# Kernel tuning notes

Measured on AMD Instinct MI355X. Metric: run time of the kernel, lower is better.

Reference implementation:

```python
import jax, jax.numpy as jnp
import numpy as np

D_MODEL = 256
N_LAYERS = 6
N_HEADS = 8
D_FF = 1024
HEAD_DIM = D_MODEL // N_HEADS
EPS = 1e-5


def layer_norm(x, scale, bias):
    mu = jnp.mean(x, axis=-1, keepdims=True)
    var = jnp.var(x, axis=-1, keepdims=True)
    return (x - mu) * jax.lax.rsqrt(var + EPS) * scale + bias


def setup_inputs() -> dict:
    key = jax.random.key(0)
    ks = jax.random.split(key, 12)
    B, T = 4, 2048
    x = jax.random.normal(ks[0], (B, T, D_MODEL), dtype=jnp.float32)
    L = N_LAYERS
    s = 0.02
    inp = {
        "x": x,
        "ln1_s": jnp.ones((L, D_MODEL), jnp.float32),
        "ln1_b": jnp.zeros((L, D_MODEL), jnp.float32),
        "wq": jax.random.normal(ks[1], (L, D_MODEL, D_MODEL), jnp.float32) * s,
        "bq": jnp.zeros((L, D_MODEL), jnp.float32),
        "wk": jax.random.normal(ks[2], (L, D_MODEL, D_MODEL), jnp.float32) * s,
        "bk": jnp.zeros((L, D_MODEL), jnp.float32),
        "wv": jax.random.normal(ks[3], (L, D_MODEL, D_MODEL), jnp.float32) * s,
        "bv": jnp.zeros((L, D_MODEL), jnp.float32),
        "wo": jax.random.normal(ks[4], (L, D_MODEL, D_MODEL), jnp.float32) * s,
        "bo": jnp.zeros((L, D_MODEL), jnp.float32),
        "ln2_s": jnp.ones((L, D_MODEL), jnp.float32),
        "ln2_b": jnp.zeros((L, D_MODEL), jnp.float32),
        "w1": jax.random.normal(ks[5], (L, D_MODEL, D_FF), jnp.float32) * s,
        "b1": jnp.zeros((L, D_FF), jnp.float32),
        "w2": jax.random.normal(ks[6], (L, D_FF, D_MODEL), jnp.float32) * s,
        "b2": jnp.zeros((L, D_MODEL), jnp.float32),
    }
    return inp


def reference(x, ln1_s, ln1_b, wq, bq, wk, bk, wv, bv, wo, bo, ln2_s, ln2_b, w1, b1, w2, b2):
    B, T, D = x.shape
    scale = 1.0 / jnp.sqrt(jnp.float32(HEAD_DIM))
    for l in range(N_LAYERS):
        normed = layer_norm(x, ln1_s[l], ln1_b[l])
        q = (normed @ wq[l] + bq[l]).reshape(B, T, N_HEADS, HEAD_DIM)
        k = (normed @ wk[l] + bk[l]).reshape(B, T, N_HEADS, HEAD_DIM)
        v = (normed @ wv[l] + bv[l]).reshape(B, T, N_HEADS, HEAD_DIM)
        scores = jnp.einsum('bqhd,bkhd->bhqk', q, k) * scale  # [B,H,T,T]
        attn = jax.nn.softmax(scores, axis=-1)
        attn_out = jnp.einsum('bhqk,bkhd->bqhd', attn, v).reshape(B, T, D)
        x = x + attn_out @ wo[l] + bo[l]
        h = layer_norm(x, ln2_s[l], ln2_b[l])
        h = jax.nn.gelu(h @ w1[l] + b1[l], approximate=False)
        x = x + h @ w2[l] + b2[l]
    return x
```

## Files before the change

### kernel.cpp

```cpp
#include <hip/hip_runtime.h>
#include <math.h>

#define D_MODELC 256
#define N_LAYERSC 6
#define N_HEADSC 8
#define D_FFC 1024
#define HEAD_DIMC 32
#define B_SZ 4
#define T_SEQ 2048
#define M_ROWS 8192
#define QKV_N 768
#define KSPLIT 2

typedef short bf16x8 __attribute__((ext_vector_type(8)));
typedef short bf16x4 __attribute__((ext_vector_type(4)));
typedef float f32x4  __attribute__((ext_vector_type(4)));
typedef unsigned u32x4 __attribute__((ext_vector_type(4)));
typedef unsigned short u16;

#define QSCALE 0.25503488f

#define SWZ(b) ((b) ^ (((b) >> 3) & 0x70))

__device__ __forceinline__ void gload16(const void* g, void* l) {
    __builtin_amdgcn_global_load_lds(
        (const __attribute__((address_space(1))) void*)g,
        (__attribute__((address_space(3))) void*)l, 16, 0, 0);
}

__device__ __forceinline__ u16 f2bf(float x) {
    unsigned u = __builtin_bit_cast(unsigned, x);
    u += 0x7FFF + ((u >> 16) & 1);
    return (u16)(u >> 16);
}

__device__ __forceinline__ float bf2f(short x) {
    return __builtin_bit_cast(float, (unsigned)((u16)x) << 16);
}

__device__ __forceinline__ unsigned pack2bf(float a, float b) {
    return __builtin_amdgcn_perm(__builtin_bit_cast(unsigned, b),
                                 __builtin_bit_cast(unsigned, a), 0x07060302u);
}

__device__ __forceinline__ float fast_gelu(float x) {
    float y  = x * 0.70710678118654752f;
    float ay = __builtin_fabsf(y);
    float t  = __builtin_amdgcn_rcpf(1.0f + 0.3275911f * ay);
    float p  = t * (0.254829592f + t * (-0.284496736f + t * (1.421413741f
               + t * (-1.453152027f + t * 1.061405429f))));
    float e  = __builtin_amdgcn_exp2f(-ay * ay * 1.4426950408889634f);
    float er = 1.0f - p * e;
    er = y < 0.0f ? -er : er;
    return 0.5f * x * (1.0f + er);
}

__device__ __forceinline__ void transpose_tile(
    const float* __restrict__ src, u16* __restrict__ dst,
    int K, int N, int k0, int n0, float scale, float (*ts)[33])
{
    const int r = threadIdx.x >> 3, c4 = (threadIdx.x & 7) * 4;
    const float4 v = *(const float4*)(src + (size_t)(k0 + r) * N + n0 + c4);
    ts[r][c4 + 0] = v.x; ts[r][c4 + 1] = v.y;
    ts[r][c4 + 2] = v.z; ts[r][c4 + 3] = v.w;
    __syncthreads();
    bf16x4 o;
#pragma unroll
    for (int i = 0; i < 4; i++) o[i] = (short)f2bf(ts[c4 + i][r] * scale);
    *(bf16x4*)(dst + (size_t)(n0 + r) * K + k0 + c4) = o;
}

__global__ __launch_bounds__(256) void prep_all(
    const float* __restrict__ wq, const float* __restrict__ wk,
    const float* __restrict__ wv, const float* __restrict__ wo,
    const float* __restrict__ w1, const float* __restrict__ w2,
    const float* __restrict__ bq, const float* __restrict__ bk,
    const float* __restrict__ bv,
    u16* __restrict__ wqkv_t, u16* __restrict__ wo_t,
    u16* __restrict__ w1_t, u16* __restrict__ w2_t,
    float* __restrict__ qkvb,
    const float* __restrict__ x, const float* __restrict__ gamma,
    const float* __restrict__ beta, float* __restrict__ X,
    u16* __restrict__ Y)
{
    __shared__ float ts[32][33];
    const int bid = blockIdx.x;
    if (bid < 1152) {
        const int sec = bid / 384, t = bid % 384;
        const int z = t >> 6, rem = t & 63, ty = rem >> 3, tx = rem & 7;
        const float* src = sec == 0 ? wq : (sec == 1 ? wk : wv);
        transpose_tile(src + (size_t)z * 65536,
                       wqkv_t + (size_t)z * QKV_N * 256 + sec * 256 * 256,
                       256, 256, ty * 32, tx * 32,
                       sec == 0 ? QSCALE : 1.0f, ts);
    } else if (bid < 1536) {
        const int t = bid - 1152;
        const int z = t >> 6, rem = t & 63, ty = rem >> 3, tx = rem & 7;
        transpose_tile(wo + (size_t)z * 65536, wo_t + (size_t)z * 65536,
                       256, 256, ty * 32, tx * 32, 1.0f, ts);
    } else if (bid < 3072) {
        const int t = bid - 1536;
        const int z = t >> 8, rem = t & 255, ty = rem >> 5, tx = rem & 31;
        transpose_tile(w1 + (size_t)z * 262144, w1_t + (size_t)z * 262144,
                       256, D_FFC, ty * 32, tx * 32, 1.0f, ts);
    } else if (bid < 4608) {
        const int t = bid - 3072;
        const int z = t >> 8, rem = t & 255, ty = rem >> 3, tx = rem & 7;
        transpose_tile(w2 + (size_t)z * 262144, w2_t + (size_t)z * 262144,
                       D_FFC, 256, ty * 32, tx * 32, 1.0f, ts);
    } else if (bid < 4626) {
        const int i = (bid - 4608) * 256 + threadIdx.x;
        const int l = i / QKV_N, j = i % QKV_N;
        float v;
        if (j < 256)      v = bq[l * 256 + j] * QSCALE;
        else if (j < 512) v = bk[l * 256 + j - 256];
        else              v = bv[l * 256 + j - 512];
        qkvb[i] = v;
    } else {
        const int w = threadIdx.x >> 6, lane = threadIdx.x & 63;
        const int row = (bid - 4626) * 4 + w;
        const float4 v = *(const float4*)(x + (size_t)row * 256 + lane * 4);
        *(float4*)(X + (size_t)row * 256 + lane * 4) = v;
        float sum = v.x + v.y + v.z + v.w;
        float sq  = v.x * v.x + v.y * v.y + v.z * v.z + v.w * v.w;
#pragma unroll
        for (int off = 32; off > 0; off >>= 1) {
            sum += __shfl_xor(sum, off, 64);
            sq  += __shfl_xor(sq,  off, 64);
        }
        float mu  = sum * (1.0f / 256.0f);
        float var = sq * (1.0f / 256.0f) - mu * mu;
        float rr  = rsqrtf(var + 1e-5f);
        const float4 g  = *(const float4*)(gamma + lane * 4);
        const float4 bb = *(const float4*)(beta + lane * 4);
        bf16x4 o;
        o[0] = (short)f2bf((v.x - mu) * rr * g.x + bb.x);
        o[1] = (short)f2bf((v.y - mu) * rr * g.y + bb.y);
        o[2] = (short)f2bf((v.z - mu) * rr * g.z + bb.z);
        o[3] = (short)f2bf((v.w - mu) * rr * g.w + bb.w);
        *(bf16x4*)(Y + (size_t)row * 256 + lane * 4) = o;
    }
}

template <int EPI>
__global__ __launch_bounds__(256) void mfma_gemm(
    const u16* __restrict__ A, const u16* __restrict__ Bt,
    const float* __restrict__ bias, u16* __restrict__ Vout,
    void* __restrict__ Cout, int N, int K)
{
    __shared__ u16 As[128 * 64];
    __shared__ u16 Bs[64 * 64];
    const int tid = threadIdx.x, w = tid >> 6, lane = tid & 63;
    const int c = lane & 15, quad = lane >> 4;
    const int row0 = blockIdx.y * 128, col0 = blockIdx.x * 64;
    const int wr = w >> 1, wc = w & 1;
    const int cswz = (c & 7) << 4;

    int flvA[4], rA[4], colA[4];
#pragma unroll
    for (int ci = 0; ci < 4; ci++) {
        flvA[ci] = (w * 4 + ci) * 1024 + lane * 16;
        const int fsw = SWZ(flvA[ci]);
        rA[ci]   = fsw >> 7;
        colA[ci] = (fsw & 127) >> 1;
    }
    int flvB[2], rB[2], colB[2];
#pragma unroll
    for (int ci = 0; ci < 2; ci++) {
        flvB[ci] = (w * 2 + ci) * 1024 + lane * 16;
        const int fsw = SWZ(flvB[ci]);
        rB[ci]   = fsw >> 7;
        colB[ci] = (fsw & 127) >> 1;
    }

    f32x4 acc[4][2] = {};

    for (int k0 = 0; k0 < K; k0 += 64) {
        __syncthreads();
#pragma unroll
        for (int ci = 0; ci < 4; ci++)
            gload16(A + (size_t)(row0 + rA[ci]) * K + k0 + colA[ci],
                    (char*)As + flvA[ci]);
#pragma unroll
        for (int ci = 0; ci < 2; ci++)
            gload16(Bt + (size_t)(col0 + rB[ci]) * K + k0 + colB[ci],
                    (char*)Bs + flvB[ci]);
        __syncthreads();
#pragma unroll
        for (int kk = 0; kk < 2; kk++) {
            bf16x8 af[4], bfv[2];
#pragma unroll
            for (int i = 0; i < 4; i++)
                af[i] = *(const bf16x8*)((const char*)As +
                    ((((wr * 64 + i * 16 + c) * 64 + kk * 32 + quad * 8) * 2) ^ cswz));
#pragma unroll
            for (int j = 0; j < 2; j++)
                bfv[j] = *(const bf16x8*)((const char*)Bs +
                    ((((wc * 32 + j * 16 + c) * 64 + kk * 32 + quad * 8) * 2) ^ cswz));
#pragma unroll
            for (int i = 0; i < 4; i++)
#pragma unroll
                for (int j = 0; j < 2; j++)
                    acc[i][j] = __builtin_amdgcn_mfma_f32_16x16x32_bf16(
                        af[i], bfv[j], acc[i][j], 0, 0, 0);
        }
    }

    float bj[2];
#pragma unroll
    for (int j = 0; j < 2; j++) bj[j] = bias[col0 + wc * 32 + j * 16 + c];

    if (EPI == 3 && col0 >= 512) {
#pragma unroll
        for (int i = 0; i < 4; i++) {
            const int tok = row0 + wr * 64 + i * 16 + quad * 4;
#pragma unroll
            for (int j = 0; j < 2; j++) {
                const int dim = col0 - 512 + wc * 32 + j * 16 + c;
                bf16x4 o;
#pragma unroll
                for (int r = 0; r < 4; r++) o[r] = (short)f2bf(acc[i][j][r] + bj[j]);
                *(bf16x4*)&Vout[(size_t)dim * M_ROWS + tok] = o;
            }
        }
        return;
    }

#pragma unroll
    for (int i = 0; i < 4; i++) {
#pragma unroll
        for (int r = 0; r < 4; r++) {
            const int gr = row0 + wr * 64 + i * 16 + quad * 4 + r;
#pragma unroll
            for (int j = 0; j < 2; j++) {
                const int gc = col0 + wc * 32 + j * 16 + c;
                float v = acc[i][j][r] + bj[j];
                if (EPI == 2) v = fast_gelu(v);
                ((u16*)Cout)[(size_t)gr * N + gc] = f2bf(v);
            }
        }
    }
}

template <int DOLN, int MERGE>
__global__ __launch_bounds__(256) void gemm_ln(
    const u16* __restrict__ A, const float* __restrict__ Lmrg,
    const u16* __restrict__ Bt, const float* __restrict__ bias,
    const float* __restrict__ resid, float* __restrict__ Xout,
    const float* __restrict__ gamma, const float* __restrict__ beta,
    u16* __restrict__ Nout, int K)
{
    __shared__ u16 As[16 * 64];
    __shared__ u16 Bs[256 * 64];
    __shared__ float2 red[4][16];
    const int tid = threadIdx.x, w = tid >> 6, lane = tid & 63;
    const int c = lane & 15, quad = lane >> 4;
    const int row0 = blockIdx.x * 16;
    const int cswz = (c & 7) << 4;

    const int flA  = tid * 16;
    const bool doA = tid < 128;
    const int fsA  = SWZ(flA);
    const int rA_m = flA >> 7, colA_m = (flA & 127) >> 1;
    const int rA_g = fsA >> 7, colA_g = (fsA & 127) >> 1;

    int flB[8], rB[8], colB[8];
#pragma unroll
    for (int ci = 0; ci < 8; ci++) {
        flB[ci]  = (w * 8 + ci) * 1024 + lane * 16;
        const int fsB = SWZ(flB[ci]);
        rB[ci]   = fsB >> 7;
        colB[ci] = (fsB & 127) >> 1;
    }

    f32x4 acc[4] = {};

    auto loadA = [&](int gc) -> bf16x8 {
        const int row = row0 + rA_m;
        const int head = gc >> 5;
        float ls = 0.f;
#pragma unroll
        for (int p = 0; p < KSPLIT; p++)
            ls += Lmrg[(size_t)p * M_ROWS * 8 + (size_t)row * 8 + head];
        const float inv = __builtin_amdgcn_rcpf(ls);
        float s[8] = {0.f, 0.f, 0.f, 0.f, 0.f, 0.f, 0.f, 0.f};
#pragma unroll
        for (int p = 0; p < KSPLIT; p++) {
            bf16x8 a = *(const bf16x8*)(A + (size_t)p * M_ROWS * 256
                                          + (size_t)row * 256 + gc);
#pragma unroll
            for (int j = 0; j < 8; j++) s[j] += bf2f(a[j]);
        }
        bf16x8 o;
#pragma unroll
        for (int j = 0; j < 8; j++) o[j] = (short)f2bf(s[j] * inv);
        return o;
    };

    bf16x8 pA;
    if (MERGE && doA) pA = loadA(colA_m);

    for (int k0 = 0; k0 < K; k0 += 64) {
        __syncthreads();
#pragma unroll
        for (int ci = 0; ci < 8; ci++)
            gload16(Bt + (size_t)rB[ci] * K + k0 + colB[ci], (char*)Bs + flB[ci]);
        if (MERGE) {
            if (doA) *(bf16x8*)((char*)As + fsA) = pA;
        } else {
            if (doA) gload16(A + (size_t)(row0 + rA_g) * K + k0 + colA_g,
                             (char*)As + flA);
        }
        __syncthreads();
        if (MERGE && doA && k0 + 64 < K)
            pA = loadA(k0 + 64 + colA_m);
#pragma unroll
        for (int kk = 0; kk < 2; kk++) {
            bf16x8 af, bfv[4];
            af = *(const bf16x8*)((const char*)As +
                (((c * 64 + kk * 32 + quad * 8) * 2) ^ cswz));
#pragma unroll
            for (int j = 0; j < 4; j++)
                bfv[j] = *(const bf16x8*)((const char*)Bs +
                    ((((w * 64 + j * 16 + c) * 64 + kk * 32 + quad * 8) * 2) ^ cswz));
#pragma unroll
            for (int j = 0; j < 4; j++)
                acc[j] = __builtin_amdgcn_mfma_f32_16x16x32_bf16(
                    af, bfv[j], acc[j], 0, 0, 0);
        }
    }

    float bj[4];
#pragma unroll
    for (int j = 0; j < 4; j++) bj[j] = bias[w * 64 + j * 16 + c];
    float xv[4][4];
#pragma unroll
    for (int r = 0; r < 4; r++) {
        const int gr = row0 + quad * 4 + r;
#pragma unroll
        for (int j = 0; j < 4; j++) {
            const int gc = w * 64 + j * 16 + c;
            xv[j][r] = acc[j][r] + bj[j] + resid[(size_t)gr * 256 + gc];
        }
    }

    if (DOLN) {
        float sm[4], sp[4];
#pragma unroll
        for (int r = 0; r < 4; r++) {
            float s = 0.f, q = 0.f;
#pragma unroll
            for (int j = 0; j < 4; j++) { s += xv[j][r]; q += xv[j][r] * xv[j][r]; }
            sm[r] = s; sp[r] = q;
        }
#pragma unroll
        for (int off = 1; off < 16; off <<= 1)
#pragma unroll
            for (int r = 0; r < 4; r++) {
                sm[r] += __shfl_xor(sm[r], off, 64);
                sp[r] += __shfl_xor(sp[r], off, 64);
            }
        __syncthreads();
        if (c == 0) {
#pragma unroll
            for (int r = 0; r < 4; r++)
                red[w][quad * 4 + r] = make_float2(sm[r], sp[r]);
        }
        __syncthreads();
#pragma unroll
        for (int r = 0; r < 4; r++) {
            const int row = quad * 4 + r;
            float2 t0 = red[0][row], t1 = red[1][row];
            float2 t2 = red[2][row], t3 = red[3][row];
            float S = (t0.x + t1.x) + (t2.x + t3.x);
            float Q = (t0.y + t1.y) + (t2.y + t3.y);
            float mu = S * (1.0f / 256.0f);
            float var = Q * (1.0f / 256.0f) - mu * mu;
            float rr = rsqrtf(var + 1e-5f);
            const int gr = row0 + row;
#pragma unroll
            for (int j = 0; j < 4; j++) {
                const int gc = w * 64 + j * 16 + c;
                float x = xv[j][r];
                Xout[(size_t)gr * 256 + gc] = x;
                Nout[(size_t)gr * 256 + gc] =
                    f2bf((x - mu) * rr * gamma[gc] + beta[gc]);
            }
        }
    } else {
#pragma unroll
        for (int r = 0; r < 4; r++) {
            const int gr = row0 + quad * 4 + r;
#pragma unroll
            for (int j = 0; j < 4; j++)
                Xout[(size_t)gr * 256 + w * 64 + j * 16 + c] = xv[j][r];
        }
    }
}

__global__ __launch_bounds__(256) void attn_kernel(
    const u16* __restrict__ QKV, const u16* __restrict__ VT,
    u16* __restrict__ PO, float* __restrict__ Lp)
{
    const int h = blockIdx.y, b = blockIdx.z;
    const int part = blockIdx.x & (KSPLIT - 1);
    const int q0 = (blockIdx.x >> 1) * 128;
    const int tid = threadIdx.x, w = tid >> 6, lane = tid & 63;
    const int c = lane & 15, quad = lane >> 4;

    __shared__ u16 Kf[2 * 4096];
    __shared__ u16 Vf[2 * 4096];

    const u16* qp = QKV + (size_t)(b * T_SEQ + q0 + w * 32 + c) * QKV_N + h * 32 + quad * 8;
    bf16x8 aQ0 = *(const bf16x8*)qp;
    bf16x8 aQ1 = *(const bf16x8*)(qp + 16 * QKV_N);

    const bf16x8 bOnes = {0x3F80, 0x3F80, 0x3F80, 0x3F80,
                          0x3F80, 0x3F80, 0x3F80, 0x3F80};

    f32x4 O[2][2] = {};
    f32x4 Ol0 = {0.f, 0.f, 0.f, 0.f}, Ol1 = {0.f, 0.f, 0.f, 0.f};

    const u16* kgp = QKV + (size_t)(b * T_SEQ + w * 16 + c) * QKV_N + 256 + h * 32 + quad * 8;
    const u16* vgp = VT + ((size_t)h * 32 + (lane & 31)) * M_ROWS + b * T_SEQ
                     + (w * 2 + (lane >> 5)) * 8;
    const int kfo = w * 512 + lane * 8;

    const int vd  = lane & 31, vdh = vd >> 4, vc = vd & 15, vhi = lane >> 5;
    const int vkh = w >> 1, vseg = w & 1;
    const int voff = ((((vkh * 2 + vdh) * 4 + 2 * vhi) * 16 + vc) * 8) + vseg * 4;

    const int kbeg = part * (T_SEQ / KSPLIT);
    const int kend = kbeg + T_SEQ / KSPLIT;

    bf16x8 gK0 = *(const bf16x8*)(kgp + (size_t)kbeg * QKV_N);
    bf16x8 gK1 = *(const bf16x8*)(kgp + (size_t)(kbeg + 64) * QKV_N);
    bf16x8 gV0 = *(const bf16x8*)(vgp + kbeg);
    bf16x8 gV1 = *(const bf16x8*)(vgp + kbeg + 64);

    int bs = 0;
    for (int k0 = kbeg; k0 < kend; k0 += 128, bs ^= 1) {
        u16* Kbuf = Kf + bs * 4096;
        u16* Vbuf = Vf + bs * 4096;
        *(bf16x8*)(Kbuf + kfo)        = gK0;
        *(bf16x8*)(Kbuf + kfo + 2048) = gK1;
        {
            bf16x4 l0v = __builtin_shufflevector(gV0, gV0, 0, 1, 2, 3);
            bf16x4 h0v = __builtin_shufflevector(gV0, gV0, 4, 5, 6, 7);
            bf16x4 l1v = __builtin_shufflevector(gV1, gV1, 0, 1, 2, 3);
            bf16x4 h1v = __builtin_shufflevector(gV1, gV1, 4, 5, 6, 7);
            *(bf16x4*)&Vbuf[voff]              = l0v;
            *(bf16x4*)&Vbuf[voff + 128]        = h0v;
            *(bf16x4*)&Vbuf[2048 + voff]       = l1v;
            *(bf16x4*)&Vbuf[2048 + voff + 128] = h1v;
        }
        __syncthreads();
        if (k0 + 128 < kend) {
            gK0 = *(const bf16x8*)(kgp + (size_t)(k0 + 128) * QKV_N);
            gK1 = *(const bf16x8*)(kgp + (size_t)(k0 + 192) * QKV_N);
            gV0 = *(const bf16x8*)(vgp + k0 + 128);
            gV1 = *(const bf16x8*)(vgp + k0 + 192);
        }

#pragma unroll
        for (int hf = 0; hf < 2; hf++) {
            const u16* Kb = Kbuf + hf * 2048;
            const u16* Vb = Vbuf + hf * 2048;

            unsigned pk0[4][2], pk1[4][2];
#pragma unroll
            for (int g = 0; g < 4; g++) {
                bf16x8 aK = *(const bf16x8*)&Kb[g * 512 + lane * 8];
                f32x4 S0 = __builtin_amdgcn_mfma_f32_16x16x32_bf16(
                    aK, aQ0, (f32x4){0.f, 0.f, 0.f, 0.f}, 0, 0, 0);
                f32x4 S1 = __builtin_amdgcn_mfma_f32_16x16x32_bf16(
                    aK, aQ1, (f32x4){0.f, 0.f, 0.f, 0.f}, 0, 0, 0);
                pk0[g][0] = pack2bf(__builtin_amdgcn_exp2f(S0[0]),
                                    __builtin_amdgcn_exp2f(S0[1]));
                pk0[g][1] = pack2bf(__builtin_amdgcn_exp2f(S0[2]),
                                    __builtin_amdgcn_exp2f(S0[3]));
                pk1[g][0] = pack2bf(__builtin_amdgcn_exp2f(S1[0]),
                                    __builtin_amdgcn_exp2f(S1[1]));
                pk1[g][1] = pack2bf(__builtin_amdgcn_exp2f(S1[2]),
                                    __builtin_amdgcn_exp2f(S1[3]));
            }

            __builtin_amdgcn_s_setprio(1);
#pragma unroll
            for (int kh = 0; kh < 2; kh++) {
                bf16x8 aP0 = __builtin_bit_cast(bf16x8,
                    (u32x4){pk0[2 * kh][0], pk0[2 * kh][1],
                            pk0[2 * kh + 1][0], pk0[2 * kh + 1][1]});
                bf16x8 aP1 = __builtin_bit_cast(bf16x8,
                    (u32x4){pk1[2 * kh][0], pk1[2 * kh][1],
                            pk1[2 * kh + 1][0], pk1[2 * kh + 1][1]});
                Ol0 = __builtin_amdgcn_mfma_f32_16x16x32_bf16(aP0, bOnes, Ol0, 0, 0, 0);
                Ol1 = __builtin_amdgcn_mfma_f32_16x16x32_bf16(aP1, bOnes, Ol1, 0, 0, 0);
#pragma unroll
                for (int dh = 0; dh < 2; dh++) {
                    bf16x8 bV = *(const bf16x8*)&Vb[((kh * 2 + dh) * 64 + lane) * 8];
                    O[0][dh] = __builtin_amdgcn_mfma_f32_16x16x32_bf16(aP0, bV, O[0][dh], 0, 0, 0);
                    O[1][dh] = __builtin_amdgcn_mfma_f32_16x16x32_bf16(aP1, bV, O[1][dh], 0, 0, 0);
                }
            }
            __builtin_amdgcn_s_setprio(0);
        }
    }

    u16* pb = PO + (size_t)part * M_ROWS * 256
              + (size_t)(b * T_SEQ + q0 + w * 32) * 256 + h * 32;
    if (c == 0) {
        float* lb = Lp + (size_t)part * M_ROWS * 8
                    + (size_t)(b * T_SEQ + q0 + w * 32) * 8 + h;
#pragma unroll
        for (int r = 0; r < 4; r++) {
            lb[(size_t)(quad * 4 + r) * 8]      = Ol0[r];
            lb[(size_t)(16 + quad * 4 + r) * 8] = Ol1[r];
        }
    }
#pragma unroll
    for (int r = 0; r < 4; r++) {
        int src = quad * 4 + r;
        pb[(size_t)src * 256 + c]             = f2bf(O[0][0][r]);
        pb[(size_t)src * 256 + 16 + c]        = f2bf(O[0][1][r]);
        pb[(size_t)(16 + src) * 256 + c]      = f2bf(O[1][0][r]);
        pb[(size_t)(16 + src) * 256 + 16 + c] = f2bf(O[1][1][r]);
    }
}

extern "C" void kernel_launch(void* const* d_in, const int* in_sizes, int n_in,
                              void* d_out, int out_size, void* d_ws, size_t ws_size,
                              hipStream_t stream)
{
    const float* x     = (const float*)d_in[0];
    const float* ln1_s = (const float*)d_in[1];
    const float* ln1_b = (const float*)d_in[2];
    const float* wq    = (const float*)d_in[3];
    const float* bq    = (const float*)d_in[4];
    const float* wk    = (const float*)d_in[5];
    const float* bk    = (const float*)d_in[6];
    const float* wv    = (const float*)d_in[7];
    const float* bv    = (const float*)d_in[8];
    const float* wo    = (const float*)d_in[9];
    const float* bo    = (const float*)d_in[10];
    const float* ln2_s = (const float*)d_in[11];
    const float* ln2_b = (const float*)d_in[12];
    const float* w1    = (const float*)d_in[13];
    const float* b1    = (const float*)d_in[14];
    const float* w2    = (const float*)d_in[15];
    const float* b2    = (const float*)d_in[16];

    float* X = (float*)d_out;

    u16* normed = (u16*)d_ws;
    u16* qkv    = normed + (size_t)M_ROWS * 256;
    u16* PO2    = qkv + (size_t)M_ROWS * QKV_N;
    u16* h1     = qkv;
    u16* wqkv_t = PO2 + (size_t)KSPLIT * M_ROWS * 256;
    u16* wo_t   = wqkv_t + (size_t)N_LAYERSC * QKV_N * 256;
    u16* w1_t   = wo_t + (size_t)N_LAYERSC * 256 * 256;
    u16* w2_t   = w1_t + (size_t)N_LAYERSC * D_FFC * 256;
    float* qkvb = (float*)(w2_t + (size_t)N_LAYERSC * 256 * D_FFC);
    u16* VTb    = (u16*)(qkvb + N_LAYERSC * QKV_N);
    float* Lp   = (float*)(VTb + (size_t)256 * M_ROWS);

    dim3 blk(256);

    prep_all<<<dim3(4626 + M_ROWS / 4), blk, 0, stream>>>(
        wq, wk, wv, wo, w1, w2, bq, bk, bv,
        wqkv_t, wo_t, w1_t, w2_t, qkvb,
        x, ln1_s, ln1_b, X, normed);

    dim3 g_qkv(QKV_N / 64, M_ROWS / 128);
    dim3 g_ff(D_FFC / 64, M_ROWS / 128);
    dim3 g_ln16(M_ROWS / 16);
    dim3 g_attn(KSPLIT * T_SEQ / 128, N_HEADSC, B_SZ);

    for (int l = 0; l < N_LAYERSC; l++) {
        mfma_gemm<3><<<g_qkv, blk, 0, stream>>>(
            normed, wqkv_t + (size_t)l * QKV_N * 256, qkvb + l * QKV_N,
            VTb, qkv, QKV_N, 256);
        attn_kernel<<<g_attn, blk, 0, stream>>>(qkv, VTb, PO2, Lp);
        gemm_ln<1, 1><<<g_ln16, blk, 0, stream>>>(
            PO2, Lp, wo_t + (size_t)l * 256 * 256, bo + l * 256, X,
            X, ln2_s + l * 256, ln2_b + l * 256, VTb, 256);
        mfma_gemm<2><<<g_ff, blk, 0, stream>>>(
            VTb, w1_t + (size_t)l * D_FFC * 256, b1 + l * D_FFC,
            nullptr, h1, D_FFC, 256);
        if (l + 1 < N_LAYERSC) {
            gemm_ln<1, 0><<<g_ln16, blk, 0, stream>>>(
                h1, nullptr, w2_t + (size_t)l * 256 * D_FFC,
                b2 + l * 256, X, X, ln1_s + (l + 1) * 256,
                ln1_b + (l + 1) * 256, normed, D_FFC);
        } else {
            gemm_ln<0, 0><<<g_ln16, blk, 0, stream>>>(
                h1, nullptr, w2_t + (size_t)l * 256 * D_FFC,
                b2 + l * 256, X, X, nullptr, nullptr, nullptr, D_FFC);
        }
    }
}
```

Before: 597.7 us.

## Double attention query tile per block to reuse K/V loads across more rows

Each attention block now handles 256 query rows instead of 128, with each wave computing four 16-row query groups instead of two. Every K/V tile staged in shared memory therefore feeds twice as many MFMAs, halving K/V global traffic and staging work per query. The cost is more accumulator and packed-probability registers per thread, which may lower occupancy, and half as many blocks in the grid (512 instead of 1024).

```diff
diff --git a/kernel.cpp b/kernel.cpp
--- a/kernel.cpp
+++ b/kernel.cpp
@@ -11,6 +11,7 @@
 #define M_ROWS 8192
 #define QKV_N 768
 #define KSPLIT 2
+#define QBLK 256
 
 typedef short bf16x8 __attribute__((ext_vector_type(8)));
 typedef short bf16x4 __attribute__((ext_vector_type(4)));
@@ -404,22 +405,24 @@
 {
     const int h = blockIdx.y, b = blockIdx.z;
     const int part = blockIdx.x & (KSPLIT - 1);
-    const int q0 = (blockIdx.x >> 1) * 128;
+    const int q0 = (blockIdx.x >> 1) * QBLK;
     const int tid = threadIdx.x, w = tid >> 6, lane = tid & 63;
     const int c = lane & 15, quad = lane >> 4;
 
     __shared__ u16 Kf[2 * 4096];
     __shared__ u16 Vf[2 * 4096];
 
-    const u16* qp = QKV + (size_t)(b * T_SEQ + q0 + w * 32 + c) * QKV_N + h * 32 + quad * 8;
-    bf16x8 aQ0 = *(const bf16x8*)qp;
-    bf16x8 aQ1 = *(const bf16x8*)(qp + 16 * QKV_N);
+    const u16* qp = QKV + (size_t)(b * T_SEQ + q0 + w * 64 + c) * QKV_N + h * 32 + quad * 8;
+    bf16x8 aQ[4];
+#pragma unroll
+    for (int qg = 0; qg < 4; qg++)
+        aQ[qg] = *(const bf16x8*)(qp + (size_t)(qg * 16) * QKV_N);
 
     const bf16x8 bOnes = {0x3F80, 0x3F80, 0x3F80, 0x3F80,
                           0x3F80, 0x3F80, 0x3F80, 0x3F80};
 
-    f32x4 O[2][2] = {};
-    f32x4 Ol0 = {0.f, 0.f, 0.f, 0.f}, Ol1 = {0.f, 0.f, 0.f, 0.f};
+    f32x4 O[4][2] = {};
+    f32x4 Ol[4] = {};
 
     const u16* kgp = QKV + (size_t)(b * T_SEQ + w * 16 + c) * QKV_N + 256 + h * 32 + quad * 8;
     const u16* vgp = VT + ((size_t)h * 32 + (lane & 31)) * M_ROWS + b * T_SEQ
@@ -467,40 +470,37 @@
             const u16* Kb = Kbuf + hf * 2048;
             const u16* Vb = Vbuf + hf * 2048;
 
-            unsigned pk0[4][2], pk1[4][2];
+            unsigned pk[4][4][2];
 #pragma unroll
             for (int g = 0; g < 4; g++) {
                 bf16x8 aK = *(const bf16x8*)&Kb[g * 512 + lane * 8];
-                f32x4 S0 = __builtin_amdgcn_mfma_f32_16x16x32_bf16(
-                    aK, aQ0, (f32x4){0.f, 0.f, 0.f, 0.f}, 0, 0, 0);
-                f32x4 S1 = __builtin_amdgcn_mfma_f32_16x16x32_bf16(
-                    aK, aQ1, (f32x4){0.f, 0.f, 0.f, 0.f}, 0, 0, 0);
-                pk0[g][0] = pack2bf(__builtin_amdgcn_exp2f(S0[0]),
-                                    __builtin_amdgcn_exp2f(S0[1]));
-                pk0[g][1] = pack2bf(__builtin_amdgcn_exp2f(S0[2]),
-                                    __builtin_amdgcn_exp2f(S0[3]));
-                pk1[g][0] = pack2bf(__builtin_amdgcn_exp2f(S1[0]),
-                                    __builtin_amdgcn_exp2f(S1[1]));
-                pk1[g][1] = pack2bf(__builtin_amdgcn_exp2f(S1[2]),
-                                    __builtin_amdgcn_exp2f(S1[3]));
+#pragma unroll
+                for (int qg = 0; qg < 4; qg++) {
+                    f32x4 S = __builtin_amdgcn_mfma_f32_16x16x32_bf16(
+                        aK, aQ[qg], (f32x4){0.f, 0.f, 0.f, 0.f}, 0, 0, 0);
+                    pk[qg][g][0] = pack2bf(__builtin_amdgcn_exp2f(S[0]),
+                                           __builtin_amdgcn_exp2f(S[1]));
+                    pk[qg][g][1] = pack2bf(__builtin_amdgcn_exp2f(S[2]),
+                                           __builtin_amdgcn_exp2f(S[3]));
+                }
             }
 
             __builtin_amdgcn_s_setprio(1);
 #pragma unroll
             for (int kh = 0; kh < 2; kh++) {
-                bf16x8 aP0 = __builtin_bit_cast(bf16x8,
-                    (u32x4){pk0[2 * kh][0], pk0[2 * kh][1],
-                            pk0[2 * kh + 1][0], pk0[2 * kh + 1][1]});
-                bf16x8 aP1 = __builtin_bit_cast(bf16x8,
-                    (u32x4){pk1[2 * kh][0], pk1[2 * kh][1],
-                            pk1[2 * kh + 1][0], pk1[2 * kh + 1][1]});
-                Ol0 = __builtin_amdgcn_mfma_f32_16x16x32_bf16(aP0, bOnes, Ol0, 0, 0, 0);
-                Ol1 = __builtin_amdgcn_mfma_f32_16x16x32_bf16(aP1, bOnes, Ol1, 0, 0, 0);
-#pragma unroll
-                for (int dh = 0; dh < 2; dh++) {
-                    bf16x8 bV = *(const bf16x8*)&Vb[((kh * 2 + dh) * 64 + lane) * 8];
-                    O[0][dh] = __builtin_amdgcn_mfma_f32_16x16x32_bf16(aP0, bV, O[0][dh], 0, 0, 0);
-                    O[1][dh] = __builtin_amdgcn_mfma_f32_16x16x32_bf16(aP1, bV, O[1][dh], 0, 0, 0);
+                bf16x8 bV0 = *(const bf16x8*)&Vb[((kh * 2 + 0) * 64 + lane) * 8];
+                bf16x8 bV1 = *(const bf16x8*)&Vb[((kh * 2 + 1) * 64 + lane) * 8];
+#pragma unroll
+                for (int qg = 0; qg < 4; qg++) {
+                    bf16x8 aP = __builtin_bit_cast(bf16x8,
+                        (u32x4){pk[qg][2 * kh][0], pk[qg][2 * kh][1],
+                                pk[qg][2 * kh + 1][0], pk[qg][2 * kh + 1][1]});
+                    Ol[qg] = __builtin_amdgcn_mfma_f32_16x16x32_bf16(
+                        aP, bOnes, Ol[qg], 0, 0, 0);
+                    O[qg][0] = __builtin_amdgcn_mfma_f32_16x16x32_bf16(
+                        aP, bV0, O[qg][0], 0, 0, 0);
+                    O[qg][1] = __builtin_amdgcn_mfma_f32_16x16x32_bf16(
+                        aP, bV1, O[qg][1], 0, 0, 0);
                 }
             }
             __builtin_amdgcn_s_setprio(0);
@@ -508,24 +508,24 @@
     }
 
     u16* pb = PO + (size_t)part * M_ROWS * 256
-              + (size_t)(b * T_SEQ + q0 + w * 32) * 256 + h * 32;
+              + (size_t)(b * T_SEQ + q0 + w * 64) * 256 + h * 32;
     if (c == 0) {
         float* lb = Lp + (size_t)part * M_ROWS * 8
-                    + (size_t)(b * T_SEQ + q0 + w * 32) * 8 + h;
+                    + (size_t)(b * T_SEQ + q0 + w * 64) * 8 + h;
+#pragma unroll
+        for (int qg = 0; qg < 4; qg++)
+#pragma unroll
+            for (int r = 0; r < 4; r++)
+                lb[(size_t)(qg * 16 + quad * 4 + r) * 8] = Ol[qg][r];
+    }
+#pragma unroll
+    for (int qg = 0; qg < 4; qg++)
 #pragma unroll
         for (int r = 0; r < 4; r++) {
-            lb[(size_t)(quad * 4 + r) * 8]      = Ol0[r];
-            lb[(size_t)(16 + quad * 4 + r) * 8] = Ol1[r];
-        }
-    }
-#pragma unroll
-    for (int r = 0; r < 4; r++) {
-        int src = quad * 4 + r;
-        pb[(size_t)src * 256 + c]             = f2bf(O[0][0][r]);
-        pb[(size_t)src * 256 + 16 + c]        = f2bf(O[0][1][r]);
-        pb[(size_t)(16 + src) * 256 + c]      = f2bf(O[1][0][r]);
-        pb[(size_t)(16 + src) * 256 + 16 + c] = f2bf(O[1][1][r]);
-    }
+            const int src = qg * 16 + quad * 4 + r;
+            pb[(size_t)src * 256 + c]      = f2bf(O[qg][0][r]);
+            pb[(size_t)src * 256 + 16 + c] = f2bf(O[qg][1][r]);
+        }
 }
 
 extern "C" void kernel_launch(void* const* d_in, const int* in_sizes, int n_in,
@@ -574,7 +574,7 @@
     dim3 g_qkv(QKV_N / 64, M_ROWS / 128);
     dim3 g_ff(D_FFC / 64, M_ROWS / 128);
     dim3 g_ln16(M_ROWS / 16);
-    dim3 g_attn(KSPLIT * T_SEQ / 128, N_HEADSC, B_SZ);
+    dim3 g_attn(KSPLIT * T_SEQ / QBLK, N_HEADSC, B_SZ);
 
     for (int l = 0; l < N_LAYERSC; l++) {
         mfma_gemm<3><<<g_qkv, blk, 0, stream>>>(
```

After: 583.1 us. 2.4% less time.
